# Kernel tuning notes

Measured on AMD Instinct MI355X. Metric: run time of the kernel, lower is better.

The kernel has to match this reference:

```python
import jax, jax.numpy as jnp
import numpy as np

N = 100000      # nodes
E = 1600000     # edges (before self-loops)
F_IN = 256      # input features
H = 8           # heads, layer 1
FH = 8          # features per head, layer 1
C = 64          # n_classes (layer 2 out, heads=1)
SLOPE = 0.2     # leaky relu negative slope


def setup_inputs() -> dict:
    key = jax.random.key(0)
    ks = jax.random.split(key, 12)
    x = jax.random.normal(ks[0], (N, F_IN), jnp.float32)
    edge_index = jax.random.randint(ks[1], (2, E), 0, N, dtype=jnp.int32)
    # scalar edge weights in [0.5, 1.5) so the (1 - 1/w) correction is well-behaved
    edge_weight = jax.random.uniform(ks[2], (E,), jnp.float32, 0.5, 1.5)
    W1 = jax.random.normal(ks[3], (F_IN, H * FH), jnp.float32) / np.sqrt(F_IN)
    att_src1 = jax.random.normal(ks[4], (H, FH), jnp.float32) * 0.1
    att_dst1 = jax.random.normal(ks[5], (H, FH), jnp.float32) * 0.1
    b1 = jnp.zeros((H * FH,), jnp.float32)
    W2 = jax.random.normal(ks[6], (H * FH, C), jnp.float32) / np.sqrt(H * FH)
    att_src2 = jax.random.normal(ks[7], (1, C), jnp.float32) * 0.1
    att_dst2 = jax.random.normal(ks[8], (1, C), jnp.float32) * 0.1
    b2 = jnp.zeros((C,), jnp.float32)
    return {"x": x, "edge_index": edge_index, "edge_weight": edge_weight,
            "W1": W1, "att_src1": att_src1, "att_dst1": att_dst1, "b1": b1,
            "W2": W2, "att_src2": att_src2, "att_dst2": att_dst2, "b2": b2}


def _gat_layer(x, src, dst, ew, W, a_src, a_dst, b, heads, fph, concat):
    n = x.shape[0]
    h = (x @ W).reshape(n, heads, fph)                      # [N,H,F]
    al_src = jnp.sum(h * a_src, axis=-1)                    # [N,H]
    al_dst = jnp.sum(h * a_dst, axis=-1)                    # [N,H]
    alpha = jax.nn.leaky_relu(al_src[src] + al_dst[dst], SLOPE)  # [E,H]
    alpha = alpha + (1.0 - 1.0 / ew)[:, None]               # scalar edge-weight correction
    # segment softmax over destination nodes
    m = jax.ops.segment_max(alpha, dst, num_segments=n)
    e = jnp.exp(alpha - m[dst])
    s = jax.ops.segment_sum(e, dst, num_segments=n)
    alpha = e / (s[dst] + 1e-16)                            # [E,H]
    msg = h[src] * alpha[:, :, None]                        # [E,H,F]
    out = jax.ops.segment_sum(msg, dst, num_segments=n)     # [N,H,F]
    out = out.reshape(n, heads * fph) if concat else out.mean(axis=1)
    return out + b


def reference(x, edge_index, edge_weight, W1, att_src1, att_dst1, b1,
              W2, att_src2, att_dst2, b2):
    n = x.shape[0]
    loops = jnp.arange(n, dtype=edge_index.dtype)
    src = jnp.concatenate([edge_index[0], loops])
    dst = jnp.concatenate([edge_index[1], loops])
    ew = jnp.concatenate([edge_weight, jnp.ones((n,), edge_weight.dtype)])  # fill_value=1.0
    # dropout layers are identity in eval mode
    h = _gat_layer(x, src, dst, ew, W1, att_src1, att_dst1, b1, H, FH, concat=True)
    h = jax.nn.elu(h)
    out = _gat_layer(h, src, dst, ew, W2, att_src2, att_dst2, b2, 1, C, concat=False)
    return out
```

## Files before the change

### kernel.cpp

```cpp
#include <hip/hip_runtime.h>
#include <math.h>

#define NNODES 100000
#define NEDGES 1600000
#define EATOT  1700000
#define FIN    256
#define C1     64
#define NH     8
#define C2     64
#define SLOPE  0.2f
#define LOG2E  1.4426950408889634f
#define QSCALE 8192.0f

#define NBKT  391
#define BCAP  5120
#define EPB_A 4096
#define NBLK_A 416

#define NT1 3125
#define NT2 1563
#define GGRID 512

typedef __attribute__((ext_vector_type(8))) short short8;
typedef __attribute__((ext_vector_type(4))) float f32x4;

__device__ __forceinline__ unsigned short f2bf(float f){
  unsigned u = __float_as_uint(f);
  unsigned r = (u + 0x7FFFu + ((u >> 16) & 1u)) >> 16;
  return (unsigned short)r;
}

__device__ __forceinline__ void splitw_body(const float* __restrict__ W,
                                            short* __restrict__ th, short* __restrict__ tl,
                                            int K, int idx){
  int k = idx >> 6, c = idx & 63;
  float w = W[idx];
  unsigned int b = __float_as_uint(w);
  unsigned short h = (unsigned short)(b >> 16);
  float hf = __uint_as_float(b & 0xffff0000u);
  float rem = w - hf;
  unsigned short lo = (unsigned short)(__float_as_uint(rem) >> 16);
  th[c * K + k] = (short)h;
  tl[c * K + k] = (short)lo;
}

__global__ void k_pre(const float* __restrict__ W1, short* __restrict__ w1h,
                      short* __restrict__ w1l, const float* __restrict__ W2,
                      short* __restrict__ w2h, short* __restrict__ w2l,
                      int* __restrict__ gcount){
  int b = blockIdx.x, t = threadIdx.x;
  if (b < 64){
    splitw_body(W1, w1h, w1l, FIN, b * 256 + t);
  } else if (b < 80){
    splitw_body(W2, w2h, w2l, C1, (b - 64) * 256 + t);
  } else {
    for (int i = t; i < NBKT; i += 256) gcount[i] = 0;
  }
}

__global__ __launch_bounds__(256) void k_bucketA(
    const int* __restrict__ ei, const float* __restrict__ ew,
    int* __restrict__ gcount, uint2* __restrict__ brec){
  __shared__ int cnt[NBKT];
  __shared__ int base[NBKT];
  int t = threadIdx.x;
  for (int i = t; i < NBKT; i += 256) cnt[i] = 0;
  __syncthreads();
  int e0 = blockIdx.x * EPB_A;
  int e1 = e0 + EPB_A; if (e1 > EATOT) e1 = EATOT;

  int dv[16]; unsigned pv[16];
  #pragma unroll
  for (int i = 0; i < 16; ++i){
    int e = e0 + t + i * 256;
    dv[i] = -1;
    if (e < e1){
      int s, d; float corr;
      if (e < NEDGES){ s = ei[e]; d = ei[NEDGES + e]; corr = 1.0f - 1.0f / ew[e]; }
      else { s = e - NEDGES; d = s; corr = 0.0f; }
      int q = __float2int_rn(corr * (LOG2E * QSCALE));
      dv[i] = d;
      pv[i] = ((unsigned)q << 17) | (unsigned)s;
      atomicAdd(&cnt[d >> 8], 1);
    }
  }
  __syncthreads();
  for (int i = t; i < NBKT; i += 256){
    int c = cnt[i];
    base[i] = c ? atomicAdd(&gcount[i], c) : 0;
    cnt[i] = 0;
  }
  __syncthreads();
  #pragma unroll
  for (int i = 0; i < 16; ++i){
    if (dv[i] >= 0){
      int bkt = dv[i] >> 8;
      int rel = base[bkt] + atomicAdd(&cnt[bkt], 1);
      brec[(size_t)bkt * BCAP + rel] = make_uint2((unsigned)dv[i], pv[i]);
    }
  }
}

__global__ void k_bucketS(const int* __restrict__ gcount, int* __restrict__ gbase,
                          int* __restrict__ rowptr){
  __shared__ int sh[512];
  int t = threadIdx.x;
  int v = (t < NBKT) ? gcount[t] : 0;
  sh[t] = v; __syncthreads();
  for (int off = 1; off < 512; off <<= 1){
    int y = (t >= off) ? sh[t - off] : 0;
    __syncthreads();
    sh[t] += y;
    __syncthreads();
  }
  if (t < NBKT) gbase[t] = sh[t] - v;
  if (t == 0) rowptr[NNODES] = EATOT;
}

__global__ __launch_bounds__(256, 2) void k_bg1(
    const uint2* __restrict__ brec, const int* __restrict__ gcount,
    const int* __restrict__ gbase, int* __restrict__ rowptr, int* __restrict__ rec,
    const float* __restrict__ X, const short* __restrict__ Bth,
    const short* __restrict__ Btl, const float* __restrict__ asrc,
    const float* __restrict__ adst, unsigned short* __restrict__ Hout,
    float* __restrict__ alsrc, float* __restrict__ aldst)
{
  __shared__ float xbuf[2][32 * 256];

  if (blockIdx.x < NBKT){
    int* hist  = (int*)&xbuf[0][0];
    int* scanb = hist + 256;
    int* excl  = scanb + 256;
    int* cur   = excl + 256;
    int bkt = blockIdx.x;
    int t = threadIdx.x;
    int n0 = bkt << 8;
    int cnt = gcount[bkt];
    int gb = gbase[bkt];
    hist[t] = 0;
    __syncthreads();
    const uint2* breg = brec + (size_t)bkt * BCAP;
    for (int j = t; j < cnt; j += 256)
      atomicAdd(&hist[breg[j].x & 255u], 1);
    __syncthreads();
    int h = hist[t];
    scanb[t] = h;
    __syncthreads();
    for (int off = 1; off < 256; off <<= 1){
      int y = (t >= off) ? scanb[t - off] : 0;
      __syncthreads();
      scanb[t] += y;
      __syncthreads();
    }
    int ex = scanb[t] - h;
    excl[t] = ex;
    cur[t] = 0;
    if (n0 + t < NNODES) rowptr[n0 + t] = gb + ex;
    __syncthreads();
    for (int j = t; j < cnt; j += 256){
      uint2 r = breg[j];
      int dl = (int)(r.x & 255u);
      int pos = gb + excl[dl] + atomicAdd(&cur[dl], 1);
      rec[pos] = (int)r.y;
    }
    return;
  }

  const int lane = threadIdx.x & 63;
  const int wave = threadIdx.x >> 6;
  const int l15 = lane & 15;
  const int kg = lane >> 4;
  const int cp = wave & 1;
  const int rh = wave >> 1;
  const int rl = rh * 16 + l15;
  const int rs = rl & 7;

  short8 bh[8][2], bl[8][2];
  #pragma unroll
  for (int ks = 0; ks < 8; ++ks){
    #pragma unroll
    for (int cc = 0; cc < 2; ++cc){
      unsigned boff = (unsigned)((cp * 2 + cc) * 16 + l15) * FIN + ks * 32 + kg * 8;
      bh[ks][cc] = *(const short8*)&Bth[boff];
      bl[ks][cc] = *(const short8*)&Btl[boff];
    }
  }
  float ascv[2], adcv[2];
  #pragma unroll
  for (int cc = 0; cc < 2; ++cc){
    ascv[cc] = asrc[(cp * 2 + cc) * 16 + l15] * LOG2E;
    adcv[cc] = adst[(cp * 2 + cc) * 16 + l15] * LOG2E;
  }

  const int t0 = blockIdx.x - NBKT;
  #pragma unroll
  for (int t = 0; t < 8; ++t){
    int r = wave * 8 + t;
    unsigned u = (unsigned)(lane ^ (r & 7));
    __builtin_amdgcn_global_load_lds(
        (const unsigned int*)(X + (size_t)(t0 * 32 + r) * FIN + u * 4),
        (unsigned int*)&xbuf[0][r * 256], 16, 0, 0);
  }

  int cur = 0;
  for (int ti = t0; ti < NT1; ti += GGRID){
    __syncthreads();
    int nxt = ti + GGRID;
    if (nxt < NT1){
      #pragma unroll
      for (int t = 0; t < 8; ++t){
        int r = wave * 8 + t;
        unsigned u = (unsigned)(lane ^ (r & 7));
        __builtin_amdgcn_global_load_lds(
            (const unsigned int*)(X + (size_t)(nxt * 32 + r) * FIN + u * 4),
            (unsigned int*)&xbuf[cur ^ 1][r * 256], 16, 0, 0);
      }
    }

    f32x4 acc[2] = {f32x4{0,0,0,0}, f32x4{0,0,0,0}};
    #pragma unroll
    for (int ks = 0; ks < 8; ++ks){
      int k0 = ks * 32 + kg * 8;
      unsigned U = (unsigned)(k0 >> 2);
      float4 xa = *(const float4*)&xbuf[cur][rl * 256 + ((U ^ rs) << 2)];
      float4 xb = *(const float4*)&xbuf[cur][rl * 256 + (((U + 1) ^ rs) << 2)];
      float xs[8] = {xa.x, xa.y, xa.z, xa.w, xb.x, xb.y, xb.z, xb.w};
      short8 ah, al;
      #pragma unroll
      for (int j = 0; j < 8; ++j){
        unsigned u = __float_as_uint(xs[j]);
        ah[j] = (short)(u >> 16);
        float hf = __uint_as_float(u & 0xffff0000u);
        al[j] = (short)(__float_as_uint(xs[j] - hf) >> 16);
      }
      #pragma unroll
      for (int cc = 0; cc < 2; ++cc){
        acc[cc] = __builtin_amdgcn_mfma_f32_16x16x32_bf16(ah, bh[ks][cc], acc[cc], 0, 0, 0);
        acc[cc] = __builtin_amdgcn_mfma_f32_16x16x32_bf16(ah, bl[ks][cc], acc[cc], 0, 0, 0);
        acc[cc] = __builtin_amdgcn_mfma_f32_16x16x32_bf16(al, bh[ks][cc], acc[cc], 0, 0, 0);
      }
    }

    int rowg = ti * 32 + rh * 16 + kg * 4;
    #pragma unroll
    for (int cc = 0; cc < 2; ++cc){
      #pragma unroll
      for (int reg = 0; reg < 4; ++reg)
        Hout[(size_t)(rowg + reg) * 64 + (cp * 2 + cc) * 16 + l15] = f2bf(acc[cc][reg]);
    }
    #pragma unroll
    for (int reg = 0; reg < 4; ++reg){
      int r = rowg + reg;
      #pragma unroll
      for (int cc = 0; cc < 2; ++cc){
        float ps = acc[cc][reg] * ascv[cc];
        float pd = acc[cc][reg] * adcv[cc];
        ps += __shfl_xor(ps, 1, 64); ps += __shfl_xor(ps, 2, 64); ps += __shfl_xor(ps, 4, 64);
        pd += __shfl_xor(pd, 1, 64); pd += __shfl_xor(pd, 2, 64); pd += __shfl_xor(pd, 4, 64);
        if ((l15 & 7) == 0){
          int head = (cp * 2 + cc) * 2 + (l15 >> 3);
          alsrc[r * NH + head] = ps;
          aldst[r * NH + head] = pd;
        }
      }
    }
    cur ^= 1;
  }
}

__global__ __launch_bounds__(256, 2) void k_gemm2(
    const unsigned short* __restrict__ Ah, const unsigned short* __restrict__ Al,
    const short* __restrict__ Bth, const short* __restrict__ Btl,
    const float* __restrict__ asrc, const float* __restrict__ adst,
    unsigned short* __restrict__ Hout, float* __restrict__ alsrc,
    float* __restrict__ aldst)
{
  __shared__ unsigned short abuf[2][2][64 * 64];
  const int lane = threadIdx.x & 63;
  const int wave = threadIdx.x >> 6;
  const int l15 = lane & 15;
  const int kg = lane >> 4;
  const int rl = wave * 16 + l15;
  const int rs = rl & 7;

  short8 bh[2][4], bl[2][4];
  #pragma unroll
  for (int ks = 0; ks < 2; ++ks){
    #pragma unroll
    for (int c = 0; c < 4; ++c){
      unsigned boff = (unsigned)(c * 16 + l15) * C1 + ks * 32 + kg * 8;
      bh[ks][c] = *(const short8*)&Bth[boff];
      bl[ks][c] = *(const short8*)&Btl[boff];
    }
  }
  float ascv[4], adcv[4];
  #pragma unroll
  for (int c = 0; c < 4; ++c){
    ascv[c] = asrc[c * 16 + l15] * LOG2E;
    adcv[c] = adst[c * 16 + l15] * LOG2E;
  }

  const int t0 = blockIdx.x;
  auto stage = [&](int buf, int tile){
    #pragma unroll
    for (int j = 0; j < 4; ++j){
      int q = wave * 4 + j;
      int p = q >> 3, rb = q & 7;
      int r = rb * 8 + (lane >> 3);
      int rg = tile * 64 + r; if (rg > NNODES - 1) rg = NNODES - 1;
      unsigned u = (unsigned)((lane & 7) ^ (lane >> 3));
      const unsigned short* src = (p ? Al : Ah) + (size_t)rg * 64 + u * 8;
      __builtin_amdgcn_global_load_lds(
          (const unsigned int*)src,
          (unsigned int*)&abuf[buf][p][rb * 512], 16, 0, 0);
    }
  };
  stage(0, t0);

  int cur = 0;
  for (int ti = t0; ti < NT2; ti += GGRID){
    __syncthreads();
    int nxt = ti + GGRID;
    if (nxt < NT2) stage(cur ^ 1, nxt);

    f32x4 acc[4] = {f32x4{0,0,0,0}, f32x4{0,0,0,0}, f32x4{0,0,0,0}, f32x4{0,0,0,0}};
    #pragma unroll
    for (int ks = 0; ks < 2; ++ks){
      unsigned U = (unsigned)(ks * 4 + kg);
      short8 ah = *(const short8*)&abuf[cur][0][rl * 64 + ((U ^ rs) << 3)];
      short8 al = *(const short8*)&abuf[cur][1][rl * 64 + ((U ^ rs) << 3)];
      #pragma unroll
      for (int c = 0; c < 4; ++c){
        acc[c] = __builtin_amdgcn_mfma_f32_16x16x32_bf16(ah, bh[ks][c], acc[c], 0, 0, 0);
        acc[c] = __builtin_amdgcn_mfma_f32_16x16x32_bf16(ah, bl[ks][c], acc[c], 0, 0, 0);
        acc[c] = __builtin_amdgcn_mfma_f32_16x16x32_bf16(al, bh[ks][c], acc[c], 0, 0, 0);
      }
    }

    int rowg = ti * 64 + wave * 16 + kg * 4;
    #pragma unroll
    for (int c = 0; c < 4; ++c){
      #pragma unroll
      for (int reg = 0; reg < 4; ++reg){
        int r = rowg + reg;
        if (r < NNODES) Hout[(size_t)r * 64 + c * 16 + l15] = f2bf(acc[c][reg]);
      }
    }
    #pragma unroll
    for (int reg = 0; reg < 4; ++reg){
      int r = rowg + reg;
      float ps = 0.0f, pd = 0.0f;
      #pragma unroll
      for (int c = 0; c < 4; ++c){
        ps = fmaf(acc[c][reg], ascv[c], ps);
        pd = fmaf(acc[c][reg], adcv[c], pd);
      }
      ps += __shfl_xor(ps, 1, 64); ps += __shfl_xor(ps, 2, 64);
      ps += __shfl_xor(ps, 4, 64); ps += __shfl_xor(ps, 8, 64);
      pd += __shfl_xor(pd, 1, 64); pd += __shfl_xor(pd, 2, 64);
      pd += __shfl_xor(pd, 4, 64); pd += __shfl_xor(pd, 8, 64);
      if (l15 == 0 && r < NNODES){ alsrc[r] = ps; aldst[r] = pd; }
    }
    cur ^= 1;
  }
}

template<int HEADS, bool DO_ELU, bool SPLIT_OUT>
__global__ __launch_bounds__(256) void k_agg(
    const int* __restrict__ rec, const int* __restrict__ rowptr,
    const unsigned short* __restrict__ hbuf,
    const float* __restrict__ alsrc, const float* __restrict__ aldst,
    const float* __restrict__ bias, float* __restrict__ outF,
    unsigned short* __restrict__ outH, unsigned short* __restrict__ outL){
  __shared__ uint2 wLds[4][64];
  int tid = blockIdx.x * blockDim.x + threadIdx.x;
  int dn = tid >> 6;
  int lane = threadIdx.x & 63;
  int w4 = (threadIdx.x >> 6) & 3;
  if (dn >= NNODES) return;
  int d = __builtin_amdgcn_readfirstlane(dn);
  int beg = rowptr[d], end = rowptr[d + 1];
  const int c = lane;
  const int hc = (HEADS == 8) ? (c >> 3) : 0;
  const int eslot = (HEADS == 8) ? (lane >> 3) : lane;
  const int hw = (HEADS == 8) ? (lane & 7) : 0;
  const int CHUNK = (HEADS == 8) ? 8 : 64;
  const unsigned cOff = (unsigned)c * 2;
  float ad_w = aldst[(size_t)d * HEADS + hw];
  float s = 0.0f, acc = 0.0f;

  for (int j0 = beg; j0 < end; j0 += CHUNK){
    int je = j0 + eslot;
    bool valid = (je < end);
    int w = rec[valid ? je : (end - 1)];
    unsigned src = (unsigned)w & 0x1FFFFu;
    float a = alsrc[src * HEADS + hw];
    float v = a + ad_w;
    v = fmaxf(v, v * SLOPE);
    v += (float)(w >> 17) * (1.0f / QSCALE);
    v = fminf(v, 60.0f);
    float e = valid ? __builtin_amdgcn_exp2f(v) : 0.0f;
    wLds[w4][lane] = make_uint2(__float_as_uint(e), src << 7);

    int rem = end - j0;
    int n8 = (HEADS == 8) ? 8 : ((rem >= 64) ? 64 : ((rem + 7) & ~7));
    for (int i0 = 0; i0 < n8; i0 += 8){
      uint2 wv[8];
      #pragma unroll
      for (int i = 0; i < 8; ++i)
        wv[i] = wLds[w4][(HEADS == 8) ? (i * 8 + hc) : (i0 + i)];
      float hv[8];
      #pragma unroll
      for (int i = 0; i < 8; ++i){
        unsigned short raw = *(const unsigned short*)((const char*)hbuf + wv[i].y + cOff);
        hv[i] = __uint_as_float((unsigned)raw << 16);
      }
      #pragma unroll
      for (int i = 0; i < 8; ++i){
        float ev = __uint_as_float(wv[i].x);
        s += ev;
        acc = fmaf(ev, hv[i], acc);
      }
    }
  }

  float o = acc / (s + 1e-16f) + bias[c];
  if (DO_ELU) o = (o > 0.0f) ? o : (__expf(o) - 1.0f);
  if (SPLIT_OUT){
    unsigned u = __float_as_uint(o);
    outH[(size_t)d * 64 + c] = (unsigned short)(u >> 16);
    float hf = __uint_as_float(u & 0xffff0000u);
    outL[(size_t)d * 64 + c] = (unsigned short)(__float_as_uint(o - hf) >> 16);
  } else {
    outF[(size_t)d * 64 + c] = o;
  }
}

extern "C" void kernel_launch(void* const* d_in, const int* in_sizes, int n_in,
                              void* d_out, int out_size, void* d_ws, size_t ws_size,
                              hipStream_t stream) {
  const float* x    = (const float*)d_in[0];
  const int*   ei   = (const int*)d_in[1];
  const float* ew   = (const float*)d_in[2];
  const float* W1   = (const float*)d_in[3];
  const float* as1  = (const float*)d_in[4];
  const float* ad1  = (const float*)d_in[5];
  const float* b1   = (const float*)d_in[6];
  const float* W2   = (const float*)d_in[7];
  const float* as2  = (const float*)d_in[8];
  const float* ad2  = (const float*)d_in[9];
  const float* b2   = (const float*)d_in[10];
  float* dout = (float*)d_out;

  float* ws = (float*)d_ws;
  size_t off = 0;
  auto alloc = [&](size_t nfloats) -> float* {
    float* p = ws + off;
    off += (nfloats + 15) & ~(size_t)15;
    return p;
  };
  unsigned short* h1 = (unsigned short*)alloc((size_t)NNODES * C1 / 2);
  unsigned short* o1h = (unsigned short*)alloc((size_t)NNODES * C1 / 2);
  unsigned short* o1l = (unsigned short*)alloc((size_t)NNODES * C1 / 2);
  float* alsrc1  = alloc((size_t)NNODES * NH);
  float* aldst1  = alloc((size_t)NNODES * NH);
  float* alsrc2  = alloc(NNODES);
  float* aldst2  = alloc(NNODES);
  int*   gcount  = (int*)alloc(NBKT + 16);
  int*   gbase   = (int*)alloc(NBKT + 16);
  int*   rowptr  = (int*)alloc(NNODES + 1);
  int*   rec     = (int*)alloc(EATOT);
  uint2* brec    = (uint2*)alloc((size_t)NBKT * BCAP * 2);
  short* wt1h    = (short*)alloc(64 * FIN / 2);
  short* wt1l    = (short*)alloc(64 * FIN / 2);
  short* wt2h    = (short*)alloc(64 * C1 / 2);
  short* wt2l    = (short*)alloc(64 * C1 / 2);
  unsigned short* h2 = h1;

  const int BS = 256;

  hipLaunchKernelGGL(k_pre, dim3(81), dim3(BS), 0, stream,
                     W1, wt1h, wt1l, W2, wt2h, wt2l, gcount);

  hipLaunchKernelGGL(k_bucketA, dim3(NBLK_A), dim3(BS), 0, stream, ei, ew, gcount, brec);
  hipLaunchKernelGGL(k_bucketS, dim3(1), dim3(512), 0, stream, gcount, gbase, rowptr);

  hipLaunchKernelGGL(k_bg1, dim3(NBKT + GGRID), dim3(BS), 0, stream,
                     brec, gcount, gbase, rowptr, rec,
                     x, wt1h, wt1l, as1, ad1, h1, alsrc1, aldst1);

  int agrid = (NNODES * 64 + BS - 1) / BS;

  hipLaunchKernelGGL((k_agg<NH, true, true>), dim3(agrid), dim3(BS), 0, stream,
                     rec, rowptr, h1, alsrc1, aldst1, b1, (float*)nullptr, o1h, o1l);

  hipLaunchKernelGGL(k_gemm2, dim3(GGRID), dim3(BS), 0, stream,
                     o1h, o1l, wt2h, wt2l, as2, ad2, h2, alsrc2, aldst2);
  hipLaunchKernelGGL((k_agg<1, false, false>), dim3(agrid), dim3(BS), 0, stream,
                     rec, rowptr, h2, alsrc2, aldst2, b2, dout,
                     (unsigned short*)nullptr, (unsigned short*)nullptr);
}
```

Measured before the change: 193.2 us.

## Fold weight split into bucket kernel and double-buffer edge weights in aggregation

```diff
diff --git a/kernel.cpp b/kernel.cpp
--- a/kernel.cpp
+++ b/kernel.cpp
@@ -44,23 +44,17 @@
   tl[c * K + k] = (short)lo;
 }
 
-__global__ void k_pre(const float* __restrict__ W1, short* __restrict__ w1h,
-                      short* __restrict__ w1l, const float* __restrict__ W2,
-                      short* __restrict__ w2h, short* __restrict__ w2l,
-                      int* __restrict__ gcount){
-  int b = blockIdx.x, t = threadIdx.x;
-  if (b < 64){
-    splitw_body(W1, w1h, w1l, FIN, b * 256 + t);
-  } else if (b < 80){
-    splitw_body(W2, w2h, w2l, C1, (b - 64) * 256 + t);
-  } else {
-    for (int i = t; i < NBKT; i += 256) gcount[i] = 0;
-  }
-}
-
 __global__ __launch_bounds__(256) void k_bucketA(
     const int* __restrict__ ei, const float* __restrict__ ew,
-    int* __restrict__ gcount, uint2* __restrict__ brec){
+    int* __restrict__ gcount, uint2* __restrict__ brec,
+    const float* __restrict__ W1, short* __restrict__ w1h, short* __restrict__ w1l,
+    const float* __restrict__ W2, short* __restrict__ w2h, short* __restrict__ w2l){
+  if (blockIdx.x >= NBLK_A){
+    int q = blockIdx.x - NBLK_A;
+    if (q < 64) splitw_body(W1, w1h, w1l, FIN, q * 256 + threadIdx.x);
+    else        splitw_body(W2, w2h, w2l, C1, (q - 64) * 256 + threadIdx.x);
+    return;
+  }
   __shared__ int cnt[NBKT];
   __shared__ int base[NBKT];
   int t = threadIdx.x;
@@ -372,7 +366,7 @@
     const float* __restrict__ alsrc, const float* __restrict__ aldst,
     const float* __restrict__ bias, float* __restrict__ outF,
     unsigned short* __restrict__ outH, unsigned short* __restrict__ outL){
-  __shared__ uint2 wLds[4][64];
+  __shared__ uint2 wLds[4][2][64];
   int tid = blockIdx.x * blockDim.x + threadIdx.x;
   int dn = tid >> 6;
   int lane = threadIdx.x & 63;
@@ -382,14 +376,13 @@
   int beg = rowptr[d], end = rowptr[d + 1];
   const int c = lane;
   const int hc = (HEADS == 8) ? (c >> 3) : 0;
-  const int eslot = (HEADS == 8) ? (lane >> 3) : lane;
+  const int eslot = lane >> 3;
   const int hw = (HEADS == 8) ? (lane & 7) : 0;
-  const int CHUNK = (HEADS == 8) ? 8 : 64;
   const unsigned cOff = (unsigned)c * 2;
   float ad_w = aldst[(size_t)d * HEADS + hw];
   float s = 0.0f, acc = 0.0f;
 
-  for (int j0 = beg; j0 < end; j0 += CHUNK){
+  auto weight_phase = [&](int j0, int slot){
     int je = j0 + eslot;
     bool valid = (je < end);
     int w = rec[valid ? je : (end - 1)];
@@ -400,28 +393,31 @@
     v += (float)(w >> 17) * (1.0f / QSCALE);
     v = fminf(v, 60.0f);
     float e = valid ? __builtin_amdgcn_exp2f(v) : 0.0f;
-    wLds[w4][lane] = make_uint2(__float_as_uint(e), src << 7);
-
-    int rem = end - j0;
-    int n8 = (HEADS == 8) ? 8 : ((rem >= 64) ? 64 : ((rem + 7) & ~7));
-    for (int i0 = 0; i0 < n8; i0 += 8){
-      uint2 wv[8];
-      #pragma unroll
-      for (int i = 0; i < 8; ++i)
-        wv[i] = wLds[w4][(HEADS == 8) ? (i * 8 + hc) : (i0 + i)];
-      float hv[8];
-      #pragma unroll
-      for (int i = 0; i < 8; ++i){
-        unsigned short raw = *(const unsigned short*)((const char*)hbuf + wv[i].y + cOff);
-        hv[i] = __uint_as_float((unsigned)raw << 16);
-      }
-      #pragma unroll
-      for (int i = 0; i < 8; ++i){
-        float ev = __uint_as_float(wv[i].x);
-        s += ev;
-        acc = fmaf(ev, hv[i], acc);
-      }
-    }
+    wLds[w4][slot][lane] = make_uint2(__float_as_uint(e), src << 7);
+  };
+
+  weight_phase(beg, 0);
+  int buf = 0;
+  for (int j0 = beg; j0 < end; j0 += 8){
+    uint2 wv[8];
+    #pragma unroll
+    for (int i = 0; i < 8; ++i)
+      wv[i] = wLds[w4][buf][i * 8 + hc];
+    float hv[8];
+    #pragma unroll
+    for (int i = 0; i < 8; ++i){
+      unsigned short raw = *(const unsigned short*)((const char*)hbuf + wv[i].y + cOff);
+      hv[i] = __uint_as_float((unsigned)raw << 16);
+    }
+    int jn = j0 + 8;
+    if (jn < end) weight_phase(jn, buf ^ 1);
+    #pragma unroll
+    for (int i = 0; i < 8; ++i){
+      float ev = __uint_as_float(wv[i].x);
+      s += ev;
+      acc = fmaf(ev, hv[i], acc);
+    }
+    buf ^= 1;
   }
 
   float o = acc / (s + 1e-16f) + bias[c];
@@ -479,10 +475,10 @@
 
   const int BS = 256;
 
-  hipLaunchKernelGGL(k_pre, dim3(81), dim3(BS), 0, stream,
-                     W1, wt1h, wt1l, W2, wt2h, wt2l, gcount);
-
-  hipLaunchKernelGGL(k_bucketA, dim3(NBLK_A), dim3(BS), 0, stream, ei, ew, gcount, brec);
+  hipMemsetAsync(gcount, 0, NBKT * sizeof(int), stream);
+
+  hipLaunchKernelGGL(k_bucketA, dim3(NBLK_A + 80), dim3(BS), 0, stream,
+                     ei, ew, gcount, brec, W1, wt1h, wt1l, W2, wt2h, wt2l);
   hipLaunchKernelGGL(k_bucketS, dim3(1), dim3(512), 0, stream, gcount, gbase, rowptr);
 
   hipLaunchKernelGGL(k_bg1, dim3(NBKT + GGRID), dim3(BS), 0, stream,
```

Measured after the change: 201.1 us. 1.04x slower.
